# Performance work log

Measured on AMD Instinct MI355X. Metric: run time of the kernel, lower is better.

The kernel has to match this reference:

```python
import jax, jax.numpy as jnp
import numpy as np

N = 32768      # nodes
E = 524288     # edges (avg degree 16)
G = 512        # graphs in batch
F_IN = 64      # one-hot node-label dim
H = 128        # hidden_dim
C = 2          # num_classes (NCI1)
BN_EPS = 1e-3  # keras BatchNormalization default epsilon


def setup_inputs() -> dict:
    key = jax.random.key(0)
    ks = jax.random.split(key, 32)
    d = {}
    d["x"] = jax.random.normal(ks[0], (N, F_IN), jnp.float32)
    d["edge_weight"] = jax.random.uniform(ks[1], (E,), jnp.float32)
    i = 2
    din = F_IN
    for l in range(5):
        d[f"W1_{l}"] = jax.random.normal(ks[i], (din, H), jnp.float32) / np.float32(np.sqrt(din)); i += 1
        d[f"b1_{l}"] = jnp.zeros((H,), jnp.float32)
        d[f"W2_{l}"] = jax.random.normal(ks[i], (H, H), jnp.float32) / np.float32(np.sqrt(H)); i += 1
        d[f"b2_{l}"] = jnp.zeros((H,), jnp.float32)
        din = H
    for j in (1, 2, 3):  # bn1, bn2, bn3 (bn0/bn4 unused in original call())
        d[f"g{j}"] = jnp.ones((H,), jnp.float32)
        d[f"be{j}"] = jnp.zeros((H,), jnp.float32)
        d[f"m{j}"] = jnp.zeros((H,), jnp.float32)
        d[f"v{j}"] = jnp.ones((H,), jnp.float32)
    d["Wm1"] = jax.random.normal(ks[i], (5 * H, 128), jnp.float32) / np.float32(np.sqrt(5 * H)); i += 1
    d["bm1"] = jnp.zeros((128,), jnp.float32)
    d["Wm2"] = jax.random.normal(ks[i], (128, C), jnp.float32) / np.float32(np.sqrt(128.0)); i += 1
    d["bm2"] = jnp.zeros((C,), jnp.float32)
    d["edge_index"] = jax.random.randint(ks[i], (2, E), 0, N, dtype=jnp.int32); i += 1
    d["node_graph_index"] = jnp.sort(jax.random.randint(ks[i], (N,), 0, G, dtype=jnp.int32))
    return d


def reference(x, edge_weight,
              W1_0, b1_0, W2_0, b2_0,
              W1_1, b1_1, W2_1, b2_1,
              W1_2, b1_2, W2_2, b2_2,
              W1_3, b1_3, W2_3, b2_3,
              W1_4, b1_4, W2_4, b2_4,
              g1, be1, m1, v1,
              g2, be2, m2, v2,
              g3, be3, m3, v3,
              Wm1, bm1, Wm2, bm2,
              edge_index, node_graph_index):
    src, dst = edge_index[0], edge_index[1]

    def gin(h, W1, b1, W2, b2):
        # GIN with eps=0: h' = MLP(h + sum_{j in N(i)} w_ij * h_j)
        msg = h[dst] * edge_weight[:, None]              # [E, d]
        agg = jax.ops.segment_sum(msg, src, num_segments=N)
        h2 = h + agg
        return jax.nn.relu(h2 @ W1 + b1) @ W2 + b2

    def bn(h, g, be, m, v):  # inference-mode batchnorm
        return (h - m) * jax.lax.rsqrt(v + BN_EPS) * g + be

    h1 = gin(x, W1_0, b1_0, W2_0, b2_0)
    h2 = gin(bn(h1, g1, be1, m1, v1), W1_1, b1_1, W2_1, b2_1)
    h3 = gin(bn(h2, g1, be1, m1, v1), W1_2, b1_2, W2_2, b2_2)  # bn1 reused, as in source
    h4 = gin(bn(h3, g2, be2, m2, v2), W1_3, b1_3, W2_3, b2_3)
    h5 = gin(bn(h4, g3, be3, m3, v3), W1_4, b1_4, W2_4, b2_4)
    h5 = bn(h5, g3, be3, m3, v3)                                # bn3 reused, as in source

    pool = lambda h: jax.ops.segment_sum(h, node_graph_index, num_segments=G)
    hg = jnp.concatenate([pool(h1), pool(h2), pool(h3), pool(h4), pool(h5)], axis=-1)  # [G, 5H]
    # readout MLP (dropout inactive at inference)
    return jax.nn.relu(hg @ Wm1 + bm1) @ Wm2 + bm2  # [G, C]
```

## Files before the change

kernel.cpp:

```cpp
#include <hip/hip_runtime.h>
#include <hip/hip_bf16.h>

#define NN 32768
#define EE 524288
#define GG 512

typedef __bf16 bf16x8 __attribute__((ext_vector_type(8)));
typedef float  f32x4  __attribute__((ext_vector_type(4)));

static __device__ __forceinline__ float bf2f(unsigned short u) {
    union { unsigned int i; float f; } v; v.i = ((unsigned int)u) << 16; return v.f;
}
static __device__ __forceinline__ unsigned short f2bf(float f) {
    __bf16 b = (__bf16)f;
    return __builtin_bit_cast(unsigned short, b);
}
static __device__ __forceinline__ unsigned int pk2(float a, float b) {
    return (unsigned int)f2bf(a) | ((unsigned int)f2bf(b) << 16);
}

struct WJob { const float* in; unsigned short* out; int K; };
struct WJobs { WJob j[10]; };

__global__ __launch_bounds__(256) void prep_kernel(WJobs jobs, const int* __restrict__ src,
                                                   int* __restrict__ cnt) {
    if (blockIdx.x < 2048) {
        int e = blockIdx.x * 256 + threadIdx.x;
        atomicAdd(&cnt[src[e]], 1);
    } else {
        int b = blockIdx.x - 2048;
        WJob jb = jobs.j[b >> 2];
        int quarter = b & 3;
        int per = jb.K * 128 / 4;
        for (int idx = quarter * per + threadIdx.x; idx < (quarter + 1) * per; idx += 256) {
            int k = idx >> 7, c = idx & 127;
            jb.out[c * jb.K + k] = f2bf(jb.in[idx]);
        }
    }
}

__global__ void scan_kernel(const int* __restrict__ cnt, int* __restrict__ row_start,
                            int* __restrict__ cursor) {
    int tid = threadIdx.x;
    int base = tid * 32;
    int vals[32];
    int s = 0;
    #pragma unroll
    for (int i = 0; i < 32; ++i) { vals[i] = cnt[base + i]; s += vals[i]; }
    int lane = tid & 63, wave = tid >> 6;
    int incl = s;
    #pragma unroll
    for (int off = 1; off < 64; off <<= 1) {
        int t = __shfl_up(incl, off);
        if (lane >= off) incl += t;
    }
    __shared__ int wave_tot[16];
    if (lane == 63) wave_tot[wave] = incl;
    __syncthreads();
    int wave_base = 0;
    for (int w = 0; w < wave; ++w) wave_base += wave_tot[w];
    int run = wave_base + incl - s;
    #pragma unroll
    for (int i = 0; i < 32; ++i) {
        row_start[base + i] = run;
        cursor[base + i] = run;
        run += vals[i];
    }
    if (tid == 1023) row_start[NN] = run;
}

__global__ void fill_kernel(const int* __restrict__ src, const int* __restrict__ dst,
                            const float* __restrict__ w,
                            int* __restrict__ cursor, unsigned int* __restrict__ csr) {
    int e = blockIdx.x * 256 + threadIdx.x;
    if (e < EE) {
        int s = src[e];
        int p = atomicAdd(&cursor[s], 1);
        csr[p] = (unsigned int)dst[e] | ((unsigned int)f2bf(w[e]) << 16);
    }
}

template<bool FIRST, bool LAST>
__global__ __launch_bounds__(256) void layer_kernel(
        const void* __restrict__ h_in,
        const int* __restrict__ row_start,
        const unsigned int* __restrict__ csr,
        const unsigned short* __restrict__ W1t,
        const float* __restrict__ b1,
        const unsigned short* __restrict__ W2t,
        const float* __restrict__ b2,
        const float* __restrict__ g, const float* __restrict__ be,
        const float* __restrict__ m, const float* __restrict__ v,
        const int* __restrict__ gidx,
        unsigned short* __restrict__ h_out,
        float* __restrict__ pools, int col_off) {

    constexpr int K1 = FIRST ? 64 : 128;
    constexpr int KS1 = K1 / 32;

    __shared__ unsigned int smem[2176];
    __shared__ float sscale[128], sshift[128];
    __shared__ int sgid[16];

    unsigned int* A1 = smem;
    unsigned int* T  = smem + 16 * 68;
    float* OUT = (float*)smem;

    int tid = threadIdx.x;
    int wave = tid >> 6, lane = tid & 63;
    int grp = lane >> 4, sub = lane & 15;
    int mrow = lane & 15, quad = lane >> 4;

    if (tid < 128) {
        float sc = g[tid] * rsqrtf(v[tid] + 1e-3f);
        sscale[tid] = sc;
        sshift[tid] = be[tid] - m[tid] * sc;
    } else if (tid < 144) {
        sgid[tid - 128] = gidx[blockIdx.x * 16 + (tid - 128)];
    }

    if (FIRST) {
        const float4* hp = (const float4*)h_in;
        for (int i = 0; i < 4; ++i) {
            int r = wave * 4 + i;
            int node = blockIdx.x * 16 + r;
            int s = row_start[node], e = row_start[node + 1];
            float ac0 = 0.f, ac1 = 0.f, ac2 = 0.f, ac3 = 0.f;
            for (int base = s; base < e; base += 64) {
                int n = e - base; if (n > 64) n = 64;
                unsigned int ev = (lane < n) ? csr[base + lane] : 0u;
                int iters = (n + 3) >> 2;
                #pragma unroll 4
                for (int t = 0; t < iters; ++t) {
                    unsigned int e2 = (unsigned int)__shfl((int)ev, 4 * t + grp);
                    float w = bf2f((unsigned short)(e2 >> 16));
                    float4 hv = hp[(e2 & 0xffffu) * 16 + sub];
                    ac0 += w * hv.x; ac1 += w * hv.y; ac2 += w * hv.z; ac3 += w * hv.w;
                }
            }
            ac0 += __shfl_xor(ac0, 16); ac0 += __shfl_xor(ac0, 32);
            ac1 += __shfl_xor(ac1, 16); ac1 += __shfl_xor(ac1, 32);
            ac2 += __shfl_xor(ac2, 16); ac2 += __shfl_xor(ac2, 32);
            ac3 += __shfl_xor(ac3, 16); ac3 += __shfl_xor(ac3, 32);
            if (grp == 0) {
                float4 self = hp[(size_t)node * 16 + sub];
                ac0 += self.x; ac1 += self.y; ac2 += self.z; ac3 += self.w;
                *(uint2*)(A1 + r * 68 + sub * 2) = make_uint2(pk2(ac0, ac1), pk2(ac2, ac3));
            }
        }
    } else {
        const uint4* hp = (const uint4*)h_in;
        for (int i = 0; i < 4; ++i) {
            int r = wave * 4 + i;
            int node = blockIdx.x * 16 + r;
            int s = row_start[node], e = row_start[node + 1];
            float acc[8];
            #pragma unroll
            for (int c = 0; c < 8; ++c) acc[c] = 0.f;
            for (int base = s; base < e; base += 64) {
                int n = e - base; if (n > 64) n = 64;
                unsigned int ev = (lane < n) ? csr[base + lane] : 0u;
                int iters = (n + 3) >> 2;
                #pragma unroll 4
                for (int t = 0; t < iters; ++t) {
                    unsigned int e2 = (unsigned int)__shfl((int)ev, 4 * t + grp);
                    float w = bf2f((unsigned short)(e2 >> 16));
                    uint4 hv = hp[(e2 & 0xffffu) * 16 + sub];
                    acc[0] += w * bf2f((unsigned short)(hv.x & 0xffff));
                    acc[1] += w * bf2f((unsigned short)(hv.x >> 16));
                    acc[2] += w * bf2f((unsigned short)(hv.y & 0xffff));
                    acc[3] += w * bf2f((unsigned short)(hv.y >> 16));
                    acc[4] += w * bf2f((unsigned short)(hv.z & 0xffff));
                    acc[5] += w * bf2f((unsigned short)(hv.z >> 16));
                    acc[6] += w * bf2f((unsigned short)(hv.w & 0xffff));
                    acc[7] += w * bf2f((unsigned short)(hv.w >> 16));
                }
            }
            #pragma unroll
            for (int c = 0; c < 8; ++c) {
                acc[c] += __shfl_xor(acc[c], 16);
                acc[c] += __shfl_xor(acc[c], 32);
            }
            if (grp == 0) {
                uint4 self = hp[(size_t)node * 16 + sub];
                acc[0] += bf2f((unsigned short)(self.x & 0xffff));
                acc[1] += bf2f((unsigned short)(self.x >> 16));
                acc[2] += bf2f((unsigned short)(self.y & 0xffff));
                acc[3] += bf2f((unsigned short)(self.y >> 16));
                acc[4] += bf2f((unsigned short)(self.z & 0xffff));
                acc[5] += bf2f((unsigned short)(self.z >> 16));
                acc[6] += bf2f((unsigned short)(self.w & 0xffff));
                acc[7] += bf2f((unsigned short)(self.w >> 16));
                *(uint4*)(A1 + r * 68 + sub * 4) =
                    make_uint4(pk2(acc[0], acc[1]), pk2(acc[2], acc[3]),
                               pk2(acc[4], acc[5]), pk2(acc[6], acc[7]));
            }
        }
    }
    __syncthreads();

    const unsigned short* A1s = (const unsigned short*)A1;
    unsigned short* Ts = (unsigned short*)T;

    bf16x8 af[KS1];
    #pragma unroll
    for (int kk = 0; kk < KS1; ++kk)
        af[kk] = *(const bf16x8*)(A1s + mrow * 136 + kk * 32 + quad * 8);

    f32x4 acc1v[2];
    #pragma unroll
    for (int c = 0; c < 2; ++c) acc1v[c] = (f32x4){0.f, 0.f, 0.f, 0.f};
    #pragma unroll
    for (int c = 0; c < 2; ++c) {
        const bf16x8* Brow = (const bf16x8*)(W1t + (size_t)(wave * 32 + c * 16 + mrow) * K1);
        #pragma unroll
        for (int kk = 0; kk < KS1; ++kk)
            acc1v[c] = __builtin_amdgcn_mfma_f32_16x16x32_bf16(af[kk], Brow[kk * 4 + quad], acc1v[c], 0, 0, 0);
    }
    #pragma unroll
    for (int c = 0; c < 2; ++c) {
        int ocol = wave * 32 + c * 16 + mrow;
        float bv = b1[ocol];
        #pragma unroll
        for (int r = 0; r < 4; ++r)
            Ts[(quad * 4 + r) * 136 + ocol] = f2bf(fmaxf(acc1v[c][r] + bv, 0.f));
    }
    __syncthreads();

    bf16x8 a2f[4];
    #pragma unroll
    for (int kk = 0; kk < 4; ++kk)
        a2f[kk] = *(const bf16x8*)(Ts + mrow * 136 + kk * 32 + quad * 8);
    f32x4 acc2v[2];
    #pragma unroll
    for (int c = 0; c < 2; ++c) acc2v[c] = (f32x4){0.f, 0.f, 0.f, 0.f};
    #pragma unroll
    for (int c = 0; c < 2; ++c) {
        const bf16x8* Brow = (const bf16x8*)(W2t + (size_t)(wave * 32 + c * 16 + mrow) * 128);
        #pragma unroll
        for (int kk = 0; kk < 4; ++kk)
            acc2v[c] = __builtin_amdgcn_mfma_f32_16x16x32_bf16(a2f[kk], Brow[kk * 4 + quad], acc2v[c], 0, 0, 0);
    }
    __syncthreads();

    #pragma unroll
    for (int c = 0; c < 2; ++c) {
        int ocol = wave * 32 + c * 16 + mrow;
        float bv = b2[ocol];
        #pragma unroll
        for (int r = 0; r < 4; ++r)
            OUT[(quad * 4 + r) * 132 + ocol] = acc2v[c][r] + bv;
    }
    __syncthreads();

    if (!LAST) {
        int row = tid >> 4, q = tid & 15;
        const float* Op = OUT + row * 132 + q * 8;
        unsigned int pk[4];
        #pragma unroll
        for (int i = 0; i < 4; ++i) {
            int c0 = q * 8 + i * 2;
            float o0 = Op[i * 2]     * sscale[c0]     + sshift[c0];
            float o1 = Op[i * 2 + 1] * sscale[c0 + 1] + sshift[c0 + 1];
            pk[i] = pk2(o0, o1);
        }
        *(uint4*)(h_out + (size_t)(blockIdx.x * 16 + row) * 128 + q * 8) =
            make_uint4(pk[0], pk[1], pk[2], pk[3]);
    }

    {
        int col = tid & 127, half = tid >> 7;
        float sc = LAST ? sscale[col] : 1.f;
        float sh = LAST ? sshift[col] : 0.f;
        float accp = 0.f;
        int cur = sgid[half * 8];
        for (int r = half * 8; r < half * 8 + 8; ++r) {
            int gi = sgid[r];
            if (gi != cur) {
                atomicAdd(&pools[(size_t)cur * 640 + col_off + col], accp);
                accp = 0.f;
                cur = gi;
            }
            float val = OUT[r * 132 + col];
            accp += LAST ? (val * sc + sh) : val;
        }
        atomicAdd(&pools[(size_t)cur * 640 + col_off + col], accp);
    }
}

__global__ __launch_bounds__(128) void readout(const float* __restrict__ pools,
                                               const float* __restrict__ Wm1,
                                               const float* __restrict__ bm1,
                                               const float* __restrict__ Wm2,
                                               const float* __restrict__ bm2,
                                               float* __restrict__ out) {
    __shared__ float row[640];
    __shared__ float partial[4];
    int gb = blockIdx.x;
    for (int k = threadIdx.x; k < 640; k += 128) row[k] = pools[(size_t)gb * 640 + k];
    __syncthreads();
    int j = threadIdx.x;
    float acc = bm1[j];
    for (int k = 0; k < 640; ++k) acc += row[k] * Wm1[(size_t)k * 128 + j];
    acc = fmaxf(acc, 0.f);
    float p0 = acc * Wm2[j * 2], p1 = acc * Wm2[j * 2 + 1];
    #pragma unroll
    for (int off = 32; off; off >>= 1) { p0 += __shfl_down(p0, off); p1 += __shfl_down(p1, off); }
    int wave = j >> 6;
    if ((j & 63) == 0) { partial[wave * 2] = p0; partial[wave * 2 + 1] = p1; }
    __syncthreads();
    if (j == 0) {
        out[gb * 2]     = bm2[0] + partial[0] + partial[2];
        out[gb * 2 + 1] = bm2[1] + partial[1] + partial[3];
    }
}

extern "C" void kernel_launch(void* const* d_in, const int* in_sizes, int n_in,
                              void* d_out, int out_size, void* d_ws, size_t ws_size,
                              hipStream_t stream) {
    const float* x  = (const float*)d_in[0];
    const float* ew = (const float*)d_in[1];
    const float *W1[5], *b1[5], *W2[5], *b2[5];
    for (int l = 0; l < 5; ++l) {
        W1[l] = (const float*)d_in[2 + 4 * l];
        b1[l] = (const float*)d_in[3 + 4 * l];
        W2[l] = (const float*)d_in[4 + 4 * l];
        b2[l] = (const float*)d_in[5 + 4 * l];
    }
    const float *bg[3], *bb[3], *bm[3], *bv[3];
    for (int j = 0; j < 3; ++j) {
        bg[j] = (const float*)d_in[22 + 4 * j];
        bb[j] = (const float*)d_in[23 + 4 * j];
        bm[j] = (const float*)d_in[24 + 4 * j];
        bv[j] = (const float*)d_in[25 + 4 * j];
    }
    const float* Wm1 = (const float*)d_in[34];
    const float* bm1 = (const float*)d_in[35];
    const float* Wm2 = (const float*)d_in[36];
    const float* bm2 = (const float*)d_in[37];
    const int* edge_index = (const int*)d_in[38];
    const int* src = edge_index;
    const int* dst = edge_index + EE;
    const int* gidx = (const int*)d_in[39];

    char* p = (char*)d_ws;
    auto alloc = [&](size_t bytes) -> void* {
        void* r = (void*)p;
        p += (bytes + 255) & ~(size_t)255;
        return r;
    };
    unsigned int* csr = (unsigned int*)alloc((size_t)EE * 4);
    int* row_start    = (int*)alloc((NN + 1) * 4);
    int* cnt          = (int*)alloc(NN * 4);
    int* cursor       = (int*)alloc(NN * 4);
    unsigned short* hA = (unsigned short*)alloc((size_t)NN * 128 * 2);
    unsigned short* hB = (unsigned short*)alloc((size_t)NN * 128 * 2);
    float* pools = (float*)alloc((size_t)GG * 640 * 4);
    unsigned short* W1t[5], *W2t[5];
    for (int l = 0; l < 5; ++l) {
        W1t[l] = (unsigned short*)alloc((size_t)128 * 128 * 2);
        W2t[l] = (unsigned short*)alloc((size_t)128 * 128 * 2);
    }

    hipMemsetAsync(cnt, 0, NN * 4, stream);
    hipMemsetAsync(pools, 0, (size_t)GG * 640 * 4, stream);

    WJobs jobs;
    for (int l = 0; l < 5; ++l) {
        jobs.j[2 * l]     = WJob{W1[l], W1t[l], (l == 0) ? 64 : 128};
        jobs.j[2 * l + 1] = WJob{W2[l], W2t[l], 128};
    }
    prep_kernel<<<2048 + 40, 256, 0, stream>>>(jobs, src, cnt);
    scan_kernel<<<1, 1024, 0, stream>>>(cnt, row_start, cursor);
    fill_kernel<<<EE / 256, 256, 0, stream>>>(src, dst, ew, cursor, csr);

    const int bnsel[5] = {0, 0, 1, 2, 2};

    layer_kernel<true, false><<<NN / 16, 256, 0, stream>>>(
        x, row_start, csr, W1t[0], b1[0], W2t[0], b2[0],
        bg[0], bb[0], bm[0], bv[0], gidx, hA, pools, 0);

    const unsigned short* hin = hA;
    unsigned short* hout = hB;
    for (int l = 1; l < 5; ++l) {
        int s = bnsel[l];
        if (l < 4) {
            layer_kernel<false, false><<<NN / 16, 256, 0, stream>>>(
                hin, row_start, csr, W1t[l], b1[l], W2t[l], b2[l],
                bg[s], bb[s], bm[s], bv[s], gidx, hout, pools, l * 128);
        } else {
            layer_kernel<false, true><<<NN / 16, 256, 0, stream>>>(
                hin, row_start, csr, W1t[l], b1[l], W2t[l], b2[l],
                bg[s], bb[s], bm[s], bv[s], gidx, hout, pools, l * 128);
        }
        unsigned short* tmp = (unsigned short*)hin;
        hin = hout;
        hout = tmp;
    }

    readout<<<GG, 128, 0, stream>>>(pools, Wm1, bm1, Wm2, bm2, (float*)d_out);
}
```

Before: 394.7 us.

## Stage block CSR segment in LDS, dual-accumulator gather, and convert x to bf16

Each block now loads its 16 nodes' contiguous CSR edge segment into shared memory once. The gather loop reads edges from LDS instead of shuffling them, and uses two independent accumulators to keep more loads in flight. The input features x are converted to bf16 in the prep kernel, which halves the gather bytes for the first layer. The cost is extra LDS use (about 8KB), a fallback path for segments longer than 2048 edges, and bf16 rounding of x.

```diff
diff --git a/kernel.cpp b/kernel.cpp
--- a/kernel.cpp
+++ b/kernel.cpp
@@ -18,16 +18,34 @@
 static __device__ __forceinline__ unsigned int pk2(float a, float b) {
     return (unsigned int)f2bf(a) | ((unsigned int)f2bf(b) << 16);
 }
+static __device__ __forceinline__ void fma8(float* a, float w, uint4 hv) {
+    a[0] += w * bf2f((unsigned short)(hv.x & 0xffff));
+    a[1] += w * bf2f((unsigned short)(hv.x >> 16));
+    a[2] += w * bf2f((unsigned short)(hv.y & 0xffff));
+    a[3] += w * bf2f((unsigned short)(hv.y >> 16));
+    a[4] += w * bf2f((unsigned short)(hv.z & 0xffff));
+    a[5] += w * bf2f((unsigned short)(hv.z >> 16));
+    a[6] += w * bf2f((unsigned short)(hv.w & 0xffff));
+    a[7] += w * bf2f((unsigned short)(hv.w >> 16));
+}
+static __device__ __forceinline__ void fma4(float* a, float w, uint2 hv) {
+    a[0] += w * bf2f((unsigned short)(hv.x & 0xffff));
+    a[1] += w * bf2f((unsigned short)(hv.x >> 16));
+    a[2] += w * bf2f((unsigned short)(hv.y & 0xffff));
+    a[3] += w * bf2f((unsigned short)(hv.y >> 16));
+}
 
 struct WJob { const float* in; unsigned short* out; int K; };
 struct WJobs { WJob j[10]; };
 
 __global__ __launch_bounds__(256) void prep_kernel(WJobs jobs, const int* __restrict__ src,
-                                                   int* __restrict__ cnt) {
+                                                   int* __restrict__ cnt,
+                                                   const float* __restrict__ x,
+                                                   unsigned short* __restrict__ xb) {
     if (blockIdx.x < 2048) {
         int e = blockIdx.x * 256 + threadIdx.x;
         atomicAdd(&cnt[src[e]], 1);
-    } else {
+    } else if (blockIdx.x < 2088) {
         int b = blockIdx.x - 2048;
         WJob jb = jobs.j[b >> 2];
         int quarter = b & 3;
@@ -35,6 +53,14 @@
         for (int idx = quarter * per + threadIdx.x; idx < (quarter + 1) * per; idx += 256) {
             int k = idx >> 7, c = idx & 127;
             jb.out[c * jb.K + k] = f2bf(jb.in[idx]);
+        }
+    } else {
+        int b2 = blockIdx.x - 2088;
+        int base = b2 * 4096 + threadIdx.x;
+        #pragma unroll
+        for (int k = 0; k < 16; ++k) {
+            int idx = base + k * 256;
+            xb[idx] = f2bf(x[idx]);
         }
     }
 }
@@ -82,7 +108,7 @@
 
 template<bool FIRST, bool LAST>
 __global__ __launch_bounds__(256) void layer_kernel(
-        const void* __restrict__ h_in,
+        const unsigned short* __restrict__ h_in,
         const int* __restrict__ row_start,
         const unsigned int* __restrict__ csr,
         const unsigned short* __restrict__ W1t,
@@ -97,9 +123,12 @@
 
     constexpr int K1 = FIRST ? 64 : 128;
     constexpr int KS1 = K1 / 32;
+    constexpr int CH = FIRST ? 4 : 8;
 
     __shared__ unsigned int smem[2176];
+    __shared__ unsigned int scsr[2048];
     __shared__ float sscale[128], sshift[128];
+    __shared__ int srow[17];
     __shared__ int sgid[16];
 
     unsigned int* A1 = smem;
@@ -117,83 +146,98 @@
         sshift[tid] = be[tid] - m[tid] * sc;
     } else if (tid < 144) {
         sgid[tid - 128] = gidx[blockIdx.x * 16 + (tid - 128)];
-    }
-
-    if (FIRST) {
-        const float4* hp = (const float4*)h_in;
-        for (int i = 0; i < 4; ++i) {
-            int r = wave * 4 + i;
-            int node = blockIdx.x * 16 + r;
-            int s = row_start[node], e = row_start[node + 1];
-            float ac0 = 0.f, ac1 = 0.f, ac2 = 0.f, ac3 = 0.f;
-            for (int base = s; base < e; base += 64) {
-                int n = e - base; if (n > 64) n = 64;
-                unsigned int ev = (lane < n) ? csr[base + lane] : 0u;
-                int iters = (n + 3) >> 2;
-                #pragma unroll 4
-                for (int t = 0; t < iters; ++t) {
-                    unsigned int e2 = (unsigned int)__shfl((int)ev, 4 * t + grp);
-                    float w = bf2f((unsigned short)(e2 >> 16));
-                    float4 hv = hp[(e2 & 0xffffu) * 16 + sub];
-                    ac0 += w * hv.x; ac1 += w * hv.y; ac2 += w * hv.z; ac3 += w * hv.w;
-                }
-            }
-            ac0 += __shfl_xor(ac0, 16); ac0 += __shfl_xor(ac0, 32);
-            ac1 += __shfl_xor(ac1, 16); ac1 += __shfl_xor(ac1, 32);
-            ac2 += __shfl_xor(ac2, 16); ac2 += __shfl_xor(ac2, 32);
-            ac3 += __shfl_xor(ac3, 16); ac3 += __shfl_xor(ac3, 32);
+    } else if (tid < 161) {
+        srow[tid - 144] = row_start[blockIdx.x * 16 + (tid - 144)];
+    }
+
+    int seg_s = row_start[blockIdx.x * 16];
+    int seg_e = row_start[blockIdx.x * 16 + 16];
+    int staged = seg_e - seg_s; if (staged > 2048) staged = 2048;
+    for (int p = tid; p < staged; p += 256) scsr[p] = csr[seg_s + p];
+    __syncthreads();
+
+    for (int i = 0; i < 4; ++i) {
+        int r = wave * 4 + i;
+        int ls = srow[r] - seg_s, le = srow[r + 1] - seg_s;
+        float accA[CH], accB[CH];
+        #pragma unroll
+        for (int c = 0; c < CH; ++c) { accA[c] = 0.f; accB[c] = 0.f; }
+
+        if (FIRST) {
+            const uint2* hp = (const uint2*)h_in;
+            int p = ls + grp;
+            if (le <= staged) {
+                for (; p + 4 < le; p += 8) {
+                    unsigned int ea = scsr[p], eb = scsr[p + 4];
+                    uint2 ha = hp[(ea & 0xffffu) * 16 + sub];
+                    uint2 hb = hp[(eb & 0xffffu) * 16 + sub];
+                    fma4(accA, bf2f((unsigned short)(ea >> 16)), ha);
+                    fma4(accB, bf2f((unsigned short)(eb >> 16)), hb);
+                }
+                if (p < le) {
+                    unsigned int ea = scsr[p];
+                    fma4(accA, bf2f((unsigned short)(ea >> 16)), hp[(ea & 0xffffu) * 16 + sub]);
+                }
+            } else {
+                for (; p < le; p += 4) {
+                    unsigned int ea = csr[seg_s + p];
+                    fma4(accA, bf2f((unsigned short)(ea >> 16)), hp[(ea & 0xffffu) * 16 + sub]);
+                }
+            }
+            #pragma unroll
+            for (int c = 0; c < 4; ++c) {
+                accA[c] += accB[c];
+                accA[c] += __shfl_xor(accA[c], 16);
+                accA[c] += __shfl_xor(accA[c], 32);
+            }
             if (grp == 0) {
-                float4 self = hp[(size_t)node * 16 + sub];
-                ac0 += self.x; ac1 += self.y; ac2 += self.z; ac3 += self.w;
-                *(uint2*)(A1 + r * 68 + sub * 2) = make_uint2(pk2(ac0, ac1), pk2(ac2, ac3));
-            }
-        }
-    } else {
-        const uint4* hp = (const uint4*)h_in;
-        for (int i = 0; i < 4; ++i) {
-            int r = wave * 4 + i;
-            int node = blockIdx.x * 16 + r;
-            int s = row_start[node], e = row_start[node + 1];
-            float acc[8];
-            #pragma unroll
-            for (int c = 0; c < 8; ++c) acc[c] = 0.f;
-            for (int base = s; base < e; base += 64) {
-                int n = e - base; if (n > 64) n = 64;
-                unsigned int ev = (lane < n) ? csr[base + lane] : 0u;
-                int iters = (n + 3) >> 2;
-                #pragma unroll 4
-                for (int t = 0; t < iters; ++t) {
-                    unsigned int e2 = (unsigned int)__shfl((int)ev, 4 * t + grp);
-                    float w = bf2f((unsigned short)(e2 >> 16));
-                    uint4 hv = hp[(e2 & 0xffffu) * 16 + sub];
-                    acc[0] += w * bf2f((unsigned short)(hv.x & 0xffff));
-                    acc[1] += w * bf2f((unsigned short)(hv.x >> 16));
-                    acc[2] += w * bf2f((unsigned short)(hv.y & 0xffff));
-                    acc[3] += w * bf2f((unsigned short)(hv.y >> 16));
-                    acc[4] += w * bf2f((unsigned short)(hv.z & 0xffff));
-                    acc[5] += w * bf2f((unsigned short)(hv.z >> 16));
-                    acc[6] += w * bf2f((unsigned short)(hv.w & 0xffff));
-                    acc[7] += w * bf2f((unsigned short)(hv.w >> 16));
+                uint2 self = hp[(size_t)(blockIdx.x * 16 + r) * 16 + sub];
+                accA[0] += bf2f((unsigned short)(self.x & 0xffff));
+                accA[1] += bf2f((unsigned short)(self.x >> 16));
+                accA[2] += bf2f((unsigned short)(self.y & 0xffff));
+                accA[3] += bf2f((unsigned short)(self.y >> 16));
+                *(uint2*)(A1 + r * 68 + sub * 2) = make_uint2(pk2(accA[0], accA[1]), pk2(accA[2], accA[3]));
+            }
+        } else {
+            const uint4* hp = (const uint4*)h_in;
+            int p = ls + grp;
+            if (le <= staged) {
+                for (; p + 4 < le; p += 8) {
+                    unsigned int ea = scsr[p], eb = scsr[p + 4];
+                    uint4 ha = hp[(ea & 0xffffu) * 16 + sub];
+                    uint4 hb = hp[(eb & 0xffffu) * 16 + sub];
+                    fma8(accA, bf2f((unsigned short)(ea >> 16)), ha);
+                    fma8(accB, bf2f((unsigned short)(eb >> 16)), hb);
+                }
+                if (p < le) {
+                    unsigned int ea = scsr[p];
+                    fma8(accA, bf2f((unsigned short)(ea >> 16)), hp[(ea & 0xffffu) * 16 + sub]);
+                }
+            } else {
+                for (; p < le; p += 4) {
+                    unsigned int ea = csr[seg_s + p];
+                    fma8(accA, bf2f((unsigned short)(ea >> 16)), hp[(ea & 0xffffu) * 16 + sub]);
                 }
             }
             #pragma unroll
             for (int c = 0; c < 8; ++c) {
-                acc[c] += __shfl_xor(acc[c], 16);
-                acc[c] += __shfl_xor(acc[c], 32);
+                accA[c] += accB[c];
+                accA[c] += __shfl_xor(accA[c], 16);
+                accA[c] += __shfl_xor(accA[c], 32);
             }
             if (grp == 0) {
-                uint4 self = hp[(size_t)node * 16 + sub];
-                acc[0] += bf2f((unsigned short)(self.x & 0xffff));
-                acc[1] += bf2f((unsigned short)(self.x >> 16));
-                acc[2] += bf2f((unsigned short)(self.y & 0xffff));
-                acc[3] += bf2f((unsigned short)(self.y >> 16));
-                acc[4] += bf2f((unsigned short)(self.z & 0xffff));
-                acc[5] += bf2f((unsigned short)(self.z >> 16));
-                acc[6] += bf2f((unsigned short)(self.w & 0xffff));
-                acc[7] += bf2f((unsigned short)(self.w >> 16));
+                uint4 self = hp[(size_t)(blockIdx.x * 16 + r) * 16 + sub];
+                accA[0] += bf2f((unsigned short)(self.x & 0xffff));
+                accA[1] += bf2f((unsigned short)(self.x >> 16));
+                accA[2] += bf2f((unsigned short)(self.y & 0xffff));
+                accA[3] += bf2f((unsigned short)(self.y >> 16));
+                accA[4] += bf2f((unsigned short)(self.z & 0xffff));
+                accA[5] += bf2f((unsigned short)(self.z >> 16));
+                accA[6] += bf2f((unsigned short)(self.w & 0xffff));
+                accA[7] += bf2f((unsigned short)(self.w >> 16));
                 *(uint4*)(A1 + r * 68 + sub * 4) =
-                    make_uint4(pk2(acc[0], acc[1]), pk2(acc[2], acc[3]),
-                               pk2(acc[4], acc[5]), pk2(acc[6], acc[7]));
+                    make_uint4(pk2(accA[0], accA[1]), pk2(accA[2], accA[3]),
+                               pk2(accA[4], accA[5]), pk2(accA[6], accA[7]));
             }
         }
     }
@@ -353,6 +397,7 @@
     int* row_start    = (int*)alloc((NN + 1) * 4);
     int* cnt          = (int*)alloc(NN * 4);
     int* cursor       = (int*)alloc(NN * 4);
+    unsigned short* xb = (unsigned short*)alloc((size_t)NN * 64 * 2);
     unsigned short* hA = (unsigned short*)alloc((size_t)NN * 128 * 2);
     unsigned short* hB = (unsigned short*)alloc((size_t)NN * 128 * 2);
     float* pools = (float*)alloc((size_t)GG * 640 * 4);
@@ -370,14 +415,14 @@
         jobs.j[2 * l]     = WJob{W1[l], W1t[l], (l == 0) ? 64 : 128};
         jobs.j[2 * l + 1] = WJob{W2[l], W2t[l], 128};
     }
-    prep_kernel<<<2048 + 40, 256, 0, stream>>>(jobs, src, cnt);
+    prep_kernel<<<2048 + 40 + 512, 256, 0, stream>>>(jobs, src, cnt, x, xb);
     scan_kernel<<<1, 1024, 0, stream>>>(cnt, row_start, cursor);
     fill_kernel<<<EE / 256, 256, 0, stream>>>(src, dst, ew, cursor, csr);
 
     const int bnsel[5] = {0, 0, 1, 2, 2};
 
     layer_kernel<true, false><<<NN / 16, 256, 0, stream>>>(
-        x, row_start, csr, W1t[0], b1[0], W2t[0], b2[0],
+        xb, row_start, csr, W1t[0], b1[0], W2t[0], b2[0],
         bg[0], bb[0], bm[0], bv[0], gidx, hA, pools, 0);
 
     const unsigned short* hin = hA;
```

Result: slower. 408.5 us (+3.5%).
